# Performance work log

Hardware: AMD Instinct MI355X
Metric: run time of the kernel (lower is better)

Reference implementation:

```python
import jax, jax.numpy as jnp
import numpy as np

B, L, D, K, C = 4, 1024, 1024, 20, 21  # images, proposals/img, feat dim, dict size, classes


def setup_inputs() -> dict:
    key = jax.random.key(0)
    ks = jax.random.split(key, 6)
    return {
        "x": jax.random.normal(ks[0], (B, L, D), jnp.float32),
        "dic": jax.random.normal(ks[1], (K, D), jnp.float32),
        "prior": jax.random.uniform(ks[2], (K,), jnp.float32),
        "Wy_w": jax.random.normal(ks[3], (C, D), jnp.float32) * 0.02,
        "Wy_b": jnp.zeros((C,), jnp.float32),
        "Wz_w": jax.random.normal(ks[4], (C, D), jnp.float32) * 0.02,
        "Wz_b": jnp.zeros((C,), jnp.float32),
        "cs_w": jax.random.normal(ks[5], (C, 2 * D), jnp.float32) * 0.01,
        "cs_b": jnp.zeros((C,), jnp.float32),
    }


def reference(x, dic, prior, Wy_w, Wy_b, Wz_w, Wz_b, cs_w, cs_b):
    # attention over a small class dictionary, then pairwise outer-sum causal logits.
    scale = 1.0 / jnp.sqrt(jnp.asarray(C, x.dtype))  # embedding_size ** 0.5 == sqrt(21)
    zd = dic @ Wz_w.T + Wz_b  # [K, C] Wz(dic), shared across images

    def per_image(y):  # y: [L, D]
        att = jax.nn.softmax(((y @ Wy_w.T + Wy_b) @ zd.T) * scale, axis=1)  # [L, K]
        # prior @ (att[:, :, None] * dic[None]) == (att * prior) @ dic
        z = (att * prior[None, :]) @ dic  # [L, D]
        # causal_score(cat(y_i, z_j)) == y_i @ W[:, :D].T + z_j @ W[:, D:].T + b
        ly = y @ cs_w[:, :D].T            # [L, C]
        lz = z @ cs_w[:, D:].T + cs_b     # [L, C]
        return (ly[:, None, :] + lz[None, :, :]).reshape(L * L, C)  # [L*L, C]

    return jax.vmap(per_image)(x)  # [B, L*L, C]
```

## Files before the change

kernel.cpp:

```cpp
#include <hip/hip_runtime.h>
#include <math.h>

#define BB 4
#define LL 1024
#define DD 1024
#define KK 20
#define CC 21
#define LC (LL * CC)
#define NQ (LC / 4)
#define XS 1032

typedef float vf4    __attribute__((ext_vector_type(4)));
typedef short bf16x8 __attribute__((ext_vector_type(8)));
typedef float f32x4  __attribute__((ext_vector_type(4)));

__device__ __forceinline__ unsigned short f2bf(float f) {
    unsigned int u = __builtin_bit_cast(unsigned int, f);
    u += 0x7FFFu + ((u >> 16) & 1u);
    return (unsigned short)(u >> 16);
}

__device__ __forceinline__ float wave_reduce_sum(float v) {
    #pragma unroll
    for (int off = 1; off < 64; off <<= 1)
        v += __shfl_xor(v, off, 64);
    return v;
}

#define DOT4(a, b) ((a).x*(b).x + (a).y*(b).y + (a).z*(b).z + (a).w*(b).w)

__global__ __launch_bounds__(64) void k0_zdM(
    const float* __restrict__ dic,
    const float* __restrict__ Wz_w, const float* __restrict__ Wz_b,
    const float* __restrict__ cs_w, const float* __restrict__ Wy_w,
    float* __restrict__ zd, float* __restrict__ M,
    unsigned short* __restrict__ Wcat)
{
    int blk = blockIdx.x;
    int lane = threadIdx.x;

    if (blk < 2 * KK * CC) {
        bool isM = (blk >= KK * CC);
        int e2 = isM ? blk - KK * CC : blk;
        int k = e2 / CC, c = e2 % CC;
        const float4* a4 = reinterpret_cast<const float4*>(dic + (size_t)k * DD);
        const float*  w  = isM ? (cs_w + (size_t)c * (2 * DD) + DD) : (Wz_w + (size_t)c * DD);
        const float4* w4 = reinterpret_cast<const float4*>(w);
        float p = 0.f;
        #pragma unroll
        for (int i = 0; i < 4; ++i) {
            float4 av = a4[lane + 64 * i];
            float4 wv = w4[lane + 64 * i];
            p += DOT4(av, wv);
        }
        p = wave_reduce_sum(p);
        if (lane == 0) {
            if (isM) M[e2] = p;
            else     zd[e2] = p + Wz_b[c];
        }
    } else {
        int e2 = blk - 2 * KK * CC;
        int base = e2 * 2048;
        #pragma unroll
        for (int t = 0; t < 32; ++t) {
            int i = base + lane + 64 * t;
            int c = i >> 10, k = i & 1023;
            float v;
            if (c < CC)          v = Wy_w[(size_t)c * DD + k];
            else if (c < 2 * CC) v = cs_w[(size_t)(c - CC) * (2 * DD) + k];
            else                 v = 0.f;
            Wcat[i] = f2bf(v);
        }
    }
}

__global__ __launch_bounds__(256) void k1_mfma(
    const float* __restrict__ x,
    const float* __restrict__ prior,
    const float* __restrict__ Wy_b, const float* __restrict__ cs_b,
    const unsigned short* __restrict__ Wcat,
    const float* __restrict__ zd, const float* __restrict__ M,
    float* __restrict__ ly_ws, float* __restrict__ lz_ws)
{
    const int tid  = threadIdx.x;
    const int wid  = tid >> 6;
    const int lane = tid & 63;
    const int fr   = lane & 15;
    const int frm  = fr & 7;
    const int kg   = lane >> 4;
    const int r0   = blockIdx.x * 8;

    __shared__ float zds[KK * CC];
    __shared__ float Ms[KK * CC];
    __shared__ float pr[KK];
    __shared__ float bias[2 * CC];
    __shared__ unsigned short xT[8 * XS];
    __shared__ float pacc[4 * 8 * 49];

    for (int i = tid; i < KK * CC; i += 256) { zds[i] = zd[i]; Ms[i] = M[i]; }
    if (tid < KK) pr[tid] = prior[tid];
    if (tid < CC) { bias[tid] = Wy_b[tid]; bias[CC + tid] = cs_b[tid]; }

    #pragma unroll
    for (int i = 0; i < 8; ++i) {
        int f = tid + i * 256;
        int row  = f >> 8;
        int col4 = f & 255;
        float4 v = *reinterpret_cast<const float4*>(x + (size_t)(r0 + row) * DD + col4 * 4);
        unsigned int lo = (unsigned int)f2bf(v.x) | ((unsigned int)f2bf(v.y) << 16);
        unsigned int hi = (unsigned int)f2bf(v.z) | ((unsigned int)f2bf(v.w) << 16);
        *reinterpret_cast<uint2*>(&xT[row * XS + col4 * 4]) = make_uint2(lo, hi);
    }
    __syncthreads();

    const int kbase = wid * 256;
    const unsigned short* w0p = Wcat + (size_t)(fr +  0) * DD + kbase + kg * 8;
    const unsigned short* w1p = Wcat + (size_t)(fr + 16) * DD + kbase + kg * 8;
    const unsigned short* w2p = Wcat + (size_t)(fr + 32) * DD + kbase + kg * 8;
    const unsigned short* ap  = &xT[frm * XS + kbase + kg * 8];

    f32x4 acc0 = {0.f, 0.f, 0.f, 0.f};
    f32x4 acc1 = {0.f, 0.f, 0.f, 0.f};
    f32x4 acc2 = {0.f, 0.f, 0.f, 0.f};

    #pragma unroll
    for (int ks = 0; ks < 8; ++ks) {
        bf16x8 af = *reinterpret_cast<const bf16x8*>(ap + ks * 32);
        bf16x8 b0 = *reinterpret_cast<const bf16x8*>(w0p + ks * 32);
        bf16x8 b1 = *reinterpret_cast<const bf16x8*>(w1p + ks * 32);
        bf16x8 b2 = *reinterpret_cast<const bf16x8*>(w2p + ks * 32);
        acc0 = __builtin_amdgcn_mfma_f32_16x16x32_bf16(af, b0, acc0, 0, 0, 0);
        acc1 = __builtin_amdgcn_mfma_f32_16x16x32_bf16(af, b1, acc1, 0, 0, 0);
        acc2 = __builtin_amdgcn_mfma_f32_16x16x32_bf16(af, b2, acc2, 0, 0, 0);
    }

    if (kg < 2) {
        #pragma unroll
        for (int j = 0; j < 4; ++j) {
            float* pw = pacc + ((wid * 8) + kg * 4 + j) * 49;
            pw[fr]      = acc0[j];
            pw[16 + fr] = acc1[j];
            pw[32 + fr] = acc2[j];
        }
    }
    __syncthreads();

    for (int o = tid; o < 384; o += 256) {
        int row = o / 48, col = o % 48;
        float s = pacc[row * 49 + col]
                + pacc[(8  + row) * 49 + col]
                + pacc[(16 + row) * 49 + col]
                + pacc[(24 + row) * 49 + col];
        pacc[row * 49 + col] = s;
    }
    __syncthreads();

    if (tid < 64) {
        const int r = tid & 7;
        const int g = tid >> 3;
        const float* f = pacc + r * 49;
        const float scale = 0.21821789023599238f;
        float s[KK];
        float m = -1e30f;
        #pragma unroll
        for (int k = 0; k < KK; ++k) {
            float t = 0.f;
            #pragma unroll
            for (int c = 0; c < CC; ++c) t += (f[c] + bias[c]) * zds[k * CC + c];
            s[k] = t * scale;
            m = fmaxf(m, s[k]);
        }
        float sum = 0.f;
        #pragma unroll
        for (int k = 0; k < KK; ++k) { s[k] = expf(s[k] - m); sum += s[k]; }
        float inv = 1.f / sum;
        float wk[KK];
        #pragma unroll
        for (int k = 0; k < KK; ++k) wk[k] = s[k] * inv * pr[k];

        size_t rr = (size_t)(r0 + r);
        for (int c = g; c < CC; c += 8) {
            float lzv = bias[CC + c];
            #pragma unroll
            for (int k = 0; k < KK; ++k) lzv += wk[k] * Ms[k * CC + c];
            ly_ws[rr * CC + c] = f[CC + c];
            lz_ws[rr * CC + c] = lzv;
        }
    }
}

__global__ __launch_bounds__(512) void k2_outer(
    const float* __restrict__ ly_ws, const float* __restrict__ lz_ws,
    float* __restrict__ out)
{
    int tid = threadIdx.x;
    int blk = blockIdx.x;
    int b  = blk >> 8;
    int i0 = (blk & 255) << 2;

    __shared__ vf4 lyp4[4 * CC];
    {
        float* lyp = reinterpret_cast<float*>(lyp4);
        if (tid < 4 * 84) {
            int i = tid / 84, f = tid % 84;
            lyp[i * 84 + f] = ly_ws[(size_t)(b * LL + i0 + i) * CC + (f % 21)];
        }
    }
    const float* lzp = lz_ws + (size_t)b * LC;
    vf4 lzv[11];
    #pragma unroll
    for (int it = 0; it < 11; ++it) {
        int idx = tid + it * 512;
        lzv[it] = (idx < NQ) ? *reinterpret_cast<const vf4*>(lzp + (size_t)idx * 4)
                             : (vf4){0.f, 0.f, 0.f, 0.f};
    }
    __syncthreads();
    int g0 = tid % 21;

    #pragma unroll
    for (int i = 0; i < 4; ++i) {
        float* op = out + (size_t)(b * LL + i0 + i) * LC;
        const vf4* lyp_i = lyp4 + i * CC;
        int g = g0;
        #pragma unroll
        for (int it = 0; it < 11; ++it) {
            int idx = tid + it * 512;
            if (idx < NQ) {
                *reinterpret_cast<vf4*>(op + (size_t)idx * 4) = lzv[it] + lyp_i[g];
            }
            g += 8; if (g >= 21) g -= 21;
        }
    }
}

extern "C" void kernel_launch(void* const* d_in, const int* in_sizes, int n_in,
                              void* d_out, int out_size, void* d_ws, size_t ws_size,
                              hipStream_t stream)
{
    const float* x     = (const float*)d_in[0];
    const float* dic   = (const float*)d_in[1];
    const float* prior = (const float*)d_in[2];
    const float* Wy_w  = (const float*)d_in[3];
    const float* Wy_b  = (const float*)d_in[4];
    const float* Wz_w  = (const float*)d_in[5];
    const float* Wz_b  = (const float*)d_in[6];
    const float* cs_w  = (const float*)d_in[7];
    const float* cs_b  = (const float*)d_in[8];
    float* out = (float*)d_out;

    float* ws = (float*)d_ws;
    float* zd = ws;
    float* M  = ws + 512;
    float* ly = ws + 1024;
    float* lz = ly + BB * LL * CC;
    unsigned short* Wcat = (unsigned short*)(ws + 1024 + 2 * BB * LL * CC);

    k0_zdM <<<dim3(2 * KK * CC + 24), dim3(64),  0, stream>>>(dic, Wz_w, Wz_b, cs_w, Wy_w,
                                                              zd, M, Wcat);
    k1_mfma<<<dim3(BB * LL / 8),      dim3(256), 0, stream>>>(x, prior, Wy_b, cs_b, Wcat,
                                                              zd, M, ly, lz);
    k2_outer<<<dim3(BB * LL / 4),     dim3(512), 0, stream>>>(ly, lz, out);
}
```

Before: 101.5 us.

## Fuse three kernels into one cooperative kernel with grid-wide syncs

Replaces the three separate launches (dictionary projections and bf16 weight packing, MFMA projection with softmax, outer-sum write) with a single cooperative kernel of 256 blocks that uses grid.sync between the phases. The goal is to remove launch gaps and inter-kernel drain between stages. In exchange the output-writing phase now runs on only 256 blocks instead of 1024, each handling 16 rows. Grid sync also adds its own cost. The old three-kernel path is kept as a fallback if the cooperative launch fails.

```diff
diff --git a/kernel.cpp b/kernel.cpp
--- a/kernel.cpp
+++ b/kernel.cpp
@@ -1,4 +1,5 @@
 #include <hip/hip_runtime.h>
+#include <hip/hip_cooperative_groups.h>
 #include <math.h>
 
 #define BB 4
@@ -10,6 +11,8 @@
 #define NQ (LC / 4)
 #define XS 1032
 
+namespace cg = cooperative_groups;
+
 typedef float vf4    __attribute__((ext_vector_type(4)));
 typedef short bf16x8 __attribute__((ext_vector_type(8)));
 typedef float f32x4  __attribute__((ext_vector_type(4)));
@@ -28,6 +31,205 @@
 }
 
 #define DOT4(a, b) ((a).x*(b).x + (a).y*(b).y + (a).z*(b).z + (a).w*(b).w)
+
+__global__ __launch_bounds__(512, 2) void fused_all(
+    const float* __restrict__ x,
+    const float* __restrict__ dic,
+    const float* __restrict__ prior,
+    const float* __restrict__ Wy_w, const float* __restrict__ Wy_b,
+    const float* __restrict__ Wz_w, const float* __restrict__ Wz_b,
+    const float* __restrict__ cs_w, const float* __restrict__ cs_b,
+    float* __restrict__ zd, float* __restrict__ M,
+    unsigned short* __restrict__ Wcat,
+    float* __restrict__ ly_ws, float* __restrict__ lz_ws,
+    float* __restrict__ out)
+{
+    cg::grid_group grid = cg::this_grid();
+
+    const int tid  = threadIdx.x;
+    const int blk  = blockIdx.x;
+    const int wid  = tid >> 6;
+    const int lane = tid & 63;
+
+    __shared__ float zds[KK * CC];
+    __shared__ float Ms[KK * CC];
+    __shared__ float pr[KK];
+    __shared__ float bias[2 * CC];
+    __shared__ unsigned short xT[16 * XS];
+    __shared__ float pacc[8 * 16 * 49];
+    __shared__ vf4 lyp4[16 * CC];
+
+    {
+        int g = blk * 8 + wid;
+        if (g < KK * CC * 2) {
+            bool isM = (g >= KK * CC);
+            int e2 = isM ? g - KK * CC : g;
+            int k = e2 / CC, c = e2 % CC;
+            const float4* a4 = reinterpret_cast<const float4*>(dic + (size_t)k * DD);
+            const float*  w  = isM ? (cs_w + (size_t)c * (2 * DD) + DD) : (Wz_w + (size_t)c * DD);
+            const float4* w4 = reinterpret_cast<const float4*>(w);
+            float p = 0.f;
+            #pragma unroll
+            for (int i = 0; i < 4; ++i) {
+                float4 av = a4[lane + 64 * i];
+                float4 wv = w4[lane + 64 * i];
+                p += DOT4(av, wv);
+            }
+            p = wave_reduce_sum(p);
+            if (lane == 0) {
+                if (isM) M[e2] = p;
+                else     zd[e2] = p + Wz_b[c];
+            }
+        } else if (g < KK * CC * 2 + 24) {
+            int e2 = g - KK * CC * 2;
+            int base = e2 * 2048;
+            #pragma unroll
+            for (int t = 0; t < 32; ++t) {
+                int i = base + lane + 64 * t;
+                int c = i >> 10, k = i & 1023;
+                float v;
+                if (c < CC)          v = Wy_w[(size_t)c * DD + k];
+                else if (c < 2 * CC) v = cs_w[(size_t)(c - CC) * (2 * DD) + k];
+                else                 v = 0.f;
+                Wcat[i] = f2bf(v);
+            }
+        }
+    }
+    __threadfence();
+    grid.sync();
+
+    {
+        const int fr = lane & 15;
+        const int kg = lane >> 4;
+        const int r0 = blk * 16;
+
+        for (int i = tid; i < KK * CC; i += 512) { zds[i] = zd[i]; Ms[i] = M[i]; }
+        if (tid < KK) pr[tid] = prior[tid];
+        if (tid < CC) { bias[tid] = Wy_b[tid]; bias[CC + tid] = cs_b[tid]; }
+
+        #pragma unroll
+        for (int i = 0; i < 8; ++i) {
+            int f = tid + i * 512;
+            int row  = f >> 8;
+            int col4 = f & 255;
+            float4 v = *reinterpret_cast<const float4*>(x + (size_t)(r0 + row) * DD + col4 * 4);
+            unsigned int lo = (unsigned int)f2bf(v.x) | ((unsigned int)f2bf(v.y) << 16);
+            unsigned int hi = (unsigned int)f2bf(v.z) | ((unsigned int)f2bf(v.w) << 16);
+            *reinterpret_cast<uint2*>(&xT[row * XS + col4 * 4]) = make_uint2(lo, hi);
+        }
+        __syncthreads();
+
+        const int kbase = wid * 128;
+        const unsigned short* w0p = Wcat + (size_t)(fr +  0) * DD + kbase + kg * 8;
+        const unsigned short* w1p = Wcat + (size_t)(fr + 16) * DD + kbase + kg * 8;
+        const unsigned short* w2p = Wcat + (size_t)(fr + 32) * DD + kbase + kg * 8;
+        const unsigned short* ap  = &xT[fr * XS + kbase + kg * 8];
+
+        f32x4 acc0 = {0.f, 0.f, 0.f, 0.f};
+        f32x4 acc1 = {0.f, 0.f, 0.f, 0.f};
+        f32x4 acc2 = {0.f, 0.f, 0.f, 0.f};
+
+        #pragma unroll
+        for (int ks = 0; ks < 4; ++ks) {
+            bf16x8 af = *reinterpret_cast<const bf16x8*>(ap + ks * 32);
+            bf16x8 b0 = *reinterpret_cast<const bf16x8*>(w0p + ks * 32);
+            bf16x8 b1 = *reinterpret_cast<const bf16x8*>(w1p + ks * 32);
+            bf16x8 b2 = *reinterpret_cast<const bf16x8*>(w2p + ks * 32);
+            acc0 = __builtin_amdgcn_mfma_f32_16x16x32_bf16(af, b0, acc0, 0, 0, 0);
+            acc1 = __builtin_amdgcn_mfma_f32_16x16x32_bf16(af, b1, acc1, 0, 0, 0);
+            acc2 = __builtin_amdgcn_mfma_f32_16x16x32_bf16(af, b2, acc2, 0, 0, 0);
+        }
+
+        #pragma unroll
+        for (int j = 0; j < 4; ++j) {
+            float* pw = pacc + ((wid * 16) + kg * 4 + j) * 49;
+            pw[fr]      = acc0[j];
+            pw[16 + fr] = acc1[j];
+            pw[32 + fr] = acc2[j];
+        }
+        __syncthreads();
+
+        for (int o = tid; o < 768; o += 512) {
+            int row = o / 48, col = o % 48;
+            float s = 0.f;
+            #pragma unroll
+            for (int w = 0; w < 8; ++w) s += pacc[((w * 16) + row) * 49 + col];
+            pacc[row * 49 + col] = s;
+        }
+        __syncthreads();
+
+        if (tid < 64) {
+            const float* f = pacc + fr * 49;
+            const float scale = 0.21821789023599238f;
+            float s[KK];
+            float m = -1e30f;
+            #pragma unroll
+            for (int k = 0; k < KK; ++k) {
+                float t = 0.f;
+                #pragma unroll
+                for (int c = 0; c < CC; ++c) t += (f[c] + bias[c]) * zds[k * CC + c];
+                s[k] = t * scale;
+                m = fmaxf(m, s[k]);
+            }
+            float sum = 0.f;
+            #pragma unroll
+            for (int k = 0; k < KK; ++k) { s[k] = expf(s[k] - m); sum += s[k]; }
+            float inv = 1.f / sum;
+            float wk[KK];
+            #pragma unroll
+            for (int k = 0; k < KK; ++k) wk[k] = s[k] * inv * pr[k];
+
+            size_t rr = (size_t)(r0 + fr);
+            for (int c = kg; c < CC; c += 4) {
+                float lzv = bias[CC + c];
+                #pragma unroll
+                for (int k = 0; k < KK; ++k) lzv += wk[k] * Ms[k * CC + c];
+                ly_ws[rr * CC + c] = f[CC + c];
+                lz_ws[rr * CC + c] = lzv;
+            }
+        }
+    }
+    __threadfence();
+    grid.sync();
+
+    {
+        const int b  = blk >> 6;
+        const int i0 = (blk & 63) << 4;
+
+        {
+            float* lyp = reinterpret_cast<float*>(lyp4);
+            for (int i2 = tid; i2 < 16 * 84; i2 += 512) {
+                int i = i2 / 84, f = i2 % 84;
+                lyp[i * 84 + f] = ly_ws[(size_t)(b * LL + i0 + i) * CC + (f % 21)];
+            }
+        }
+        const float* lzp = lz_ws + (size_t)b * LC;
+        vf4 lzv[11];
+        #pragma unroll
+        for (int it = 0; it < 11; ++it) {
+            int idx = tid + it * 512;
+            lzv[it] = (idx < NQ) ? *reinterpret_cast<const vf4*>(lzp + (size_t)idx * 4)
+                                 : (vf4){0.f, 0.f, 0.f, 0.f};
+        }
+        __syncthreads();
+        int g0 = tid % 21;
+
+        #pragma unroll
+        for (int i = 0; i < 16; ++i) {
+            float* op = out + (size_t)(b * LL + i0 + i) * LC;
+            const vf4* lyp_i = lyp4 + i * CC;
+            int g = g0;
+            #pragma unroll
+            for (int it = 0; it < 11; ++it) {
+                int idx = tid + it * 512;
+                if (idx < NQ) {
+                    *reinterpret_cast<vf4*>(op + (size_t)idx * 4) = lzv[it] + lyp_i[g];
+                }
+                g += 8; if (g >= 21) g -= 21;
+            }
+        }
+    }
+}
 
 __global__ __launch_bounds__(64) void k0_zdM(
     const float* __restrict__ dic,
@@ -255,9 +457,20 @@
     float* lz = ly + BB * LL * CC;
     unsigned short* Wcat = (unsigned short*)(ws + 1024 + 2 * BB * LL * CC);
 
-    k0_zdM <<<dim3(2 * KK * CC + 24), dim3(64),  0, stream>>>(dic, Wz_w, Wz_b, cs_w, Wy_w,
-                                                              zd, M, Wcat);
-    k1_mfma<<<dim3(BB * LL / 8),      dim3(256), 0, stream>>>(x, prior, Wy_b, cs_b, Wcat,
-                                                              zd, M, ly, lz);
-    k2_outer<<<dim3(BB * LL / 4),     dim3(512), 0, stream>>>(ly, lz, out);
-}
+    void* args[] = {
+        (void*)&x, (void*)&dic, (void*)&prior,
+        (void*)&Wy_w, (void*)&Wy_b, (void*)&Wz_w, (void*)&Wz_b,
+        (void*)&cs_w, (void*)&cs_b,
+        (void*)&zd, (void*)&M, (void*)&Wcat,
+        (void*)&ly, (void*)&lz, (void*)&out
+    };
+    hipError_t err = hipLaunchCooperativeKernel((void*)fused_all, dim3(256), dim3(512),
+                                                args, 0, stream);
+    if (err != hipSuccess) {
+        k0_zdM <<<dim3(2 * KK * CC + 24), dim3(64),  0, stream>>>(dic, Wz_w, Wz_b, cs_w, Wy_w,
+                                                                  zd, M, Wcat);
+        k1_mfma<<<dim3(BB * LL / 8),      dim3(256), 0, stream>>>(x, prior, Wy_b, cs_b, Wcat,
+                                                                  zd, M, ly, lz);
+        k2_outer<<<dim3(BB * LL / 4),     dim3(512), 0, stream>>>(ly, lz, out);
+    }
+}
```

Result: slower. 218.5 us (+115.2%).
